# Kernel optimization log

Measured on AMD Instinct MI355X. Metric: run time of the kernel, lower is better.

The kernel has to match this reference:

```python
import jax, jax.numpy as jnp
import numpy as np

ALPHA = 0.2  # LeakyReLU negative slope
NEG_INF = -9e15


def setup_inputs() -> dict:
    key = jax.random.key(0)
    k1, k2, k3, k4 = jax.random.split(key, 4)
    B, T, N, F_in, F_out = 8, 8, 1024, 64, 64
    h = jax.random.normal(k1, (B, T, N, F_in), dtype=jnp.float32)
    adj = jax.random.randint(k2, (B, T, N, N), 0, 2, dtype=jnp.int32)
    # xavier_uniform with gain=1.414
    def xavier(k, shape, gain=1.414):
        fan_in, fan_out = shape[0], shape[1]
        bound = gain * np.sqrt(6.0 / (fan_in + fan_out))
        return jax.random.uniform(k, shape, jnp.float32, -bound, bound)
    W = xavier(k3, (F_in, F_out))
    a = xavier(k4, (2 * F_out, 1))
    return {"h": h, "adj": adj, "W": W, "a": a}


def reference(h, adj, W, a):
    # h: [B,T,N,F_in], adj: [B,T,N,N], W: [F_in,F_out], a: [2*F_out,1]
    F_out = W.shape[1]
    Wh = h @ W  # [B,T,N,F_out]
    a1 = a[:F_out, 0]   # source half
    a2 = a[F_out:, 0]   # target half
    s1 = Wh @ a1        # [B,T,N]
    s2 = Wh @ a2        # [B,T,N]
    # e[...,i,j] = LeakyReLU(s1_i + s2_j)  == original concat-linear score
    e = jax.nn.leaky_relu(s1[..., :, None] + s2[..., None, :], negative_slope=ALPHA)
    att = jnp.where(adj > 0, e, NEG_INF)
    att = jax.nn.softmax(att, axis=-1)  # [B,T,N,N]
    # dropout omitted: reference runs in eval mode (p only active in training)
    h_prime = att @ Wh  # [B,T,N,F_out]
    return jax.nn.elu(h_prime)  # concat=True path
```

## Files before the change

### kernel.cpp

```cpp
#include <hip/hip_runtime.h>

#define NN 1024
#define FF 64
#define NBT 64

typedef float f32x4 __attribute__((ext_vector_type(4)));
typedef short s16x8 __attribute__((ext_vector_type(8)));

__device__ __forceinline__ short f2bf(float f) {
    unsigned u = __builtin_bit_cast(unsigned, f);
    u = (u + 0x7FFFu + ((u >> 16) & 1u)) >> 16;
    return (short)u;
}

__global__ __launch_bounds__(256) void k1(const float* __restrict__ h,
                                          const float* __restrict__ W,
                                          const float* __restrict__ a,
                                          short* __restrict__ WhT,
                                          float* __restrict__ s1g,
                                          float* __restrict__ s2g) {
    __shared__ float Wl[64 * 64];
    __shared__ float al[128];
    __shared__ float s1sh[128], s2sh[128];
    const int blk = blockIdx.x;
    const int bt = blk >> 3;
    const int rbase = (blk & 7) * 128;
    const int t = threadIdx.x;

    for (int i = t; i < 1024; i += 256)
        ((f32x4*)Wl)[i] = ((const f32x4*)W)[i];
    if (t < 32) ((f32x4*)al)[t] = ((const f32x4*)a)[t];
    __syncthreads();

    const int row = rbase + (t & 127);
    const int half = t >> 7;
    const float* hrow = h + ((size_t)bt * NN + row) * FF;
    float hv[64];
#pragma unroll
    for (int i = 0; i < 16; i++)
        ((f32x4*)hv)[i] = ((const f32x4*)hrow)[i];

    float s1 = 0.f, s2 = 0.f;
    short* wt = WhT + (size_t)bt * FF * NN + row;
#pragma unroll
    for (int cgi = 0; cgi < 8; cgi++) {
        const int cg = half * 8 + cgi;
        f32x4 acc = {0.f, 0.f, 0.f, 0.f};
#pragma unroll
        for (int k = 0; k < 64; k++) {
            f32x4 w4 = ((const f32x4*)Wl)[k * 16 + cg];
            acc += hv[k] * w4;
        }
        const int c0 = cg * 4;
        s1 += acc.x * al[c0] + acc.y * al[c0 + 1] + acc.z * al[c0 + 2] + acc.w * al[c0 + 3];
        s2 += acc.x * al[64 + c0] + acc.y * al[64 + c0 + 1] + acc.z * al[64 + c0 + 2] + acc.w * al[64 + c0 + 3];
        wt[(size_t)(c0 + 0) * NN] = f2bf(acc.x);
        wt[(size_t)(c0 + 1) * NN] = f2bf(acc.y);
        wt[(size_t)(c0 + 2) * NN] = f2bf(acc.z);
        wt[(size_t)(c0 + 3) * NN] = f2bf(acc.w);
    }
    if (half == 1) { s1sh[t & 127] = s1; s2sh[t & 127] = s2; }
    __syncthreads();
    if (half == 0) {
        s1g[bt * NN + row] = s1 + s1sh[t];
        s2g[bt * NN + row] = s2 + s2sh[t];
    }
}

__global__ __launch_bounds__(256) void k2(const int* __restrict__ adj,
                                          const short* __restrict__ WhT,
                                          const float* __restrict__ s1g,
                                          const float* __restrict__ s2g,
                                          float* __restrict__ out) {
    __shared__ __align__(16) short Pa[64 * 40];
    __shared__ __align__(16) short Pw[64 * 40];
    __shared__ float s2l[NN];
    __shared__ float rsum[64];

    const int bx = blockIdx.x;
    const int bt = bx >> 4;
    const int ibase = (bx & 15) * 64;
    const int t = threadIdx.x;

    ((f32x4*)s2l)[t] = ((const f32x4*)(s2g + bt * NN))[t];

    const int r = t >> 2;
    const int jc = (t & 3) * 8;
    const float s1v = s1g[bt * NN + ibase + r];
    float rs = 0.f;

    const int* adjp = adj + ((size_t)bt * NN + ibase + r) * NN + jc;
    const short* whp = WhT + (size_t)bt * FF * NN + (size_t)r * NN + jc;

    const int wv = t >> 6;
    const int l = t & 63;
    const int m = l & 15;
    const int q = l >> 4;
    const s16x8* aptr = (const s16x8*)&Pa[(wv * 16 + m) * 40 + q * 8];
    const s16x8* bp0 = (const s16x8*)&Pw[(0 * 16 + m) * 40 + q * 8];
    const s16x8* bp1 = (const s16x8*)&Pw[(1 * 16 + m) * 40 + q * 8];
    const s16x8* bp2 = (const s16x8*)&Pw[(2 * 16 + m) * 40 + q * 8];
    const s16x8* bp3 = (const s16x8*)&Pw[(3 * 16 + m) * 40 + q * 8];

    f32x4 acc0 = {0.f, 0.f, 0.f, 0.f};
    f32x4 acc1 = {0.f, 0.f, 0.f, 0.f};
    f32x4 acc2 = {0.f, 0.f, 0.f, 0.f};
    f32x4 acc3 = {0.f, 0.f, 0.f, 0.f};

    int4 ca0 = *(const int4*)(adjp);
    int4 ca1 = *(const int4*)(adjp + 4);
    int4 cw  = *(const int4*)(whp);

    __syncthreads();

    for (int jt = 0; jt < 32; jt++) {
        const int jn = (jt < 31) ? jt + 1 : 31;
        int4 na0 = *(const int4*)(adjp + jn * 32);
        int4 na1 = *(const int4*)(adjp + jn * 32 + 4);
        int4 nw  = *(const int4*)(whp + jn * 32);

        int aj[8] = {ca0.x, ca0.y, ca0.z, ca0.w, ca1.x, ca1.y, ca1.z, ca1.w};
        f32x4 s2a = *(const f32x4*)&s2l[jt * 32 + jc];
        f32x4 s2b = *(const f32x4*)&s2l[jt * 32 + jc + 4];
        float sv[8] = {s2a.x, s2a.y, s2a.z, s2a.w, s2b.x, s2b.y, s2b.z, s2b.w};
        s16x8 pbv;
#pragma unroll
        for (int u = 0; u < 8; u++) {
            float e = s1v + sv[u];
            e = e > 0.f ? e : 0.2f * e;
            e = fminf(e, 60.f);
            float p = (aj[u] > 0) ? __expf(e) : 0.f;
            rs += p;
            pbv[u] = f2bf(p);
        }
        *(s16x8*)&Pa[r * 40 + jc] = pbv;
        *(int4*)&Pw[r * 40 + jc] = cw;
        __syncthreads();

        s16x8 af = *aptr;
        acc0 = __builtin_amdgcn_mfma_f32_16x16x32_bf16(af, *bp0, acc0, 0, 0, 0);
        acc1 = __builtin_amdgcn_mfma_f32_16x16x32_bf16(af, *bp1, acc1, 0, 0, 0);
        acc2 = __builtin_amdgcn_mfma_f32_16x16x32_bf16(af, *bp2, acc2, 0, 0, 0);
        acc3 = __builtin_amdgcn_mfma_f32_16x16x32_bf16(af, *bp3, acc3, 0, 0, 0);
        __syncthreads();

        ca0 = na0; ca1 = na1; cw = nw;
    }

    rs += __shfl_xor(rs, 1);
    rs += __shfl_xor(rs, 2);
    if ((t & 3) == 0) rsum[r] = rs;
    __syncthreads();

    float rinv[4];
#pragma unroll
    for (int e = 0; e < 4; e++) {
        float rv = rsum[wv * 16 + q * 4 + e];
        rinv[e] = rv > 0.f ? 1.f / rv : 0.f;
    }
    float* outp = out + ((size_t)bt * NN + ibase + wv * 16 + q * 4) * FF + m;
#pragma unroll
    for (int e = 0; e < 4; e++) {
        float v0 = acc0[e] * rinv[e];
        float v1 = acc1[e] * rinv[e];
        float v2 = acc2[e] * rinv[e];
        float v3 = acc3[e] * rinv[e];
        v0 = v0 > 0.f ? v0 : expm1f(v0);
        v1 = v1 > 0.f ? v1 : expm1f(v1);
        v2 = v2 > 0.f ? v2 : expm1f(v2);
        v3 = v3 > 0.f ? v3 : expm1f(v3);
        float* o = outp + (size_t)e * FF;
        o[0]  = v0;
        o[16] = v1;
        o[32] = v2;
        o[48] = v3;
    }
}

extern "C" void kernel_launch(void* const* d_in, const int* in_sizes, int n_in,
                              void* d_out, int out_size, void* d_ws, size_t ws_size,
                              hipStream_t stream) {
    const float* h  = (const float*)d_in[0];
    const int*  adj = (const int*)d_in[1];
    const float* W  = (const float*)d_in[2];
    const float* a  = (const float*)d_in[3];
    float* out = (float*)d_out;

    short* WhT = (short*)d_ws;
    float* s1  = (float*)((char*)d_ws + (size_t)NBT * FF * NN * 2);
    float* s2  = s1 + NBT * NN;

    k1<<<512, 256, 0, stream>>>(h, W, a, WhT, s1, s2);
    k2<<<1024, 256, 0, stream>>>(adj, WhT, s1, s2, out);
}
```

Measured before the change: 415.7 us.

## Load MFMA operands directly into registers, removing LDS staging and barriers

Each lane now computes its attention probabilities directly in the MFMA A-operand layout and loads its WhT B-fragments straight from global memory. This removes the shared-memory staging of P and Wh and the two block barriers per iteration, and the row sums are reduced with wave shuffles instead of through LDS. In exchange, each wave now loads all 64 columns of Wh itself, four times the previous Wh traffic. The adj loads are now strided by row per lane, which may coalesce worse.

New measurement: 421.0 us. No clear change (+1.3%).

```diff
diff --git a/kernel.cpp b/kernel.cpp
--- a/kernel.cpp
+++ b/kernel.cpp
@@ -72,90 +72,80 @@
                                           const float* __restrict__ s1g,
                                           const float* __restrict__ s2g,
                                           float* __restrict__ out) {
-    __shared__ __align__(16) short Pa[64 * 40];
-    __shared__ __align__(16) short Pw[64 * 40];
     __shared__ float s2l[NN];
-    __shared__ float rsum[64];
 
     const int bx = blockIdx.x;
     const int bt = bx >> 4;
     const int ibase = (bx & 15) * 64;
     const int t = threadIdx.x;
-
-    ((f32x4*)s2l)[t] = ((const f32x4*)(s2g + bt * NN))[t];
-
-    const int r = t >> 2;
-    const int jc = (t & 3) * 8;
-    const float s1v = s1g[bt * NN + ibase + r];
-    float rs = 0.f;
-
-    const int* adjp = adj + ((size_t)bt * NN + ibase + r) * NN + jc;
-    const short* whp = WhT + (size_t)bt * FF * NN + (size_t)r * NN + jc;
-
     const int wv = t >> 6;
     const int l = t & 63;
     const int m = l & 15;
     const int q = l >> 4;
-    const s16x8* aptr = (const s16x8*)&Pa[(wv * 16 + m) * 40 + q * 8];
-    const s16x8* bp0 = (const s16x8*)&Pw[(0 * 16 + m) * 40 + q * 8];
-    const s16x8* bp1 = (const s16x8*)&Pw[(1 * 16 + m) * 40 + q * 8];
-    const s16x8* bp2 = (const s16x8*)&Pw[(2 * 16 + m) * 40 + q * 8];
-    const s16x8* bp3 = (const s16x8*)&Pw[(3 * 16 + m) * 40 + q * 8];
+
+    ((f32x4*)s2l)[t] = ((const f32x4*)(s2g + (size_t)bt * NN))[t];
+
+    const int row = ibase + wv * 16 + m;
+    const float s1v = s1g[bt * NN + row];
+
+    const int* adjp = adj + ((size_t)bt * NN + row) * NN + q * 8;
+    const short* whp = WhT + (size_t)bt * FF * NN + (size_t)m * NN + q * 8;
 
     f32x4 acc0 = {0.f, 0.f, 0.f, 0.f};
     f32x4 acc1 = {0.f, 0.f, 0.f, 0.f};
     f32x4 acc2 = {0.f, 0.f, 0.f, 0.f};
     f32x4 acc3 = {0.f, 0.f, 0.f, 0.f};
+    float rs = 0.f;
 
     int4 ca0 = *(const int4*)(adjp);
     int4 ca1 = *(const int4*)(adjp + 4);
-    int4 cw  = *(const int4*)(whp);
+    s16x8 cb0 = *(const s16x8*)(whp);
+    s16x8 cb1 = *(const s16x8*)(whp + 16 * NN);
+    s16x8 cb2 = *(const s16x8*)(whp + 32 * NN);
+    s16x8 cb3 = *(const s16x8*)(whp + 48 * NN);
 
     __syncthreads();
 
     for (int jt = 0; jt < 32; jt++) {
-        const int jn = (jt < 31) ? jt + 1 : 31;
-        int4 na0 = *(const int4*)(adjp + jn * 32);
-        int4 na1 = *(const int4*)(adjp + jn * 32 + 4);
-        int4 nw  = *(const int4*)(whp + jn * 32);
+        const int jn = (jt < 31) ? (jt + 1) * 32 : 31 * 32;
+        int4 na0 = *(const int4*)(adjp + jn);
+        int4 na1 = *(const int4*)(adjp + jn + 4);
+        s16x8 nb0 = *(const s16x8*)(whp + jn);
+        s16x8 nb1 = *(const s16x8*)(whp + 16 * NN + jn);
+        s16x8 nb2 = *(const s16x8*)(whp + 32 * NN + jn);
+        s16x8 nb3 = *(const s16x8*)(whp + 48 * NN + jn);
 
+        f32x4 s2a = *(const f32x4*)&s2l[jt * 32 + q * 8];
+        f32x4 s2b = *(const f32x4*)&s2l[jt * 32 + q * 8 + 4];
         int aj[8] = {ca0.x, ca0.y, ca0.z, ca0.w, ca1.x, ca1.y, ca1.z, ca1.w};
-        f32x4 s2a = *(const f32x4*)&s2l[jt * 32 + jc];
-        f32x4 s2b = *(const f32x4*)&s2l[jt * 32 + jc + 4];
         float sv[8] = {s2a.x, s2a.y, s2a.z, s2a.w, s2b.x, s2b.y, s2b.z, s2b.w};
-        s16x8 pbv;
+        s16x8 af;
 #pragma unroll
         for (int u = 0; u < 8; u++) {
             float e = s1v + sv[u];
-            e = e > 0.f ? e : 0.2f * e;
+            e = fmaxf(e, 0.2f * e);
             e = fminf(e, 60.f);
             float p = (aj[u] > 0) ? __expf(e) : 0.f;
             rs += p;
-            pbv[u] = f2bf(p);
+            af[u] = f2bf(p);
         }
-        *(s16x8*)&Pa[r * 40 + jc] = pbv;
-        *(int4*)&Pw[r * 40 + jc] = cw;
-        __syncthreads();
 
-        s16x8 af = *aptr;
-        acc0 = __builtin_amdgcn_mfma_f32_16x16x32_bf16(af, *bp0, acc0, 0, 0, 0);
-        acc1 = __builtin_amdgcn_mfma_f32_16x16x32_bf16(af, *bp1, acc1, 0, 0, 0);
-        acc2 = __builtin_amdgcn_mfma_f32_16x16x32_bf16(af, *bp2, acc2, 0, 0, 0);
-        acc3 = __builtin_amdgcn_mfma_f32_16x16x32_bf16(af, *bp3, acc3, 0, 0, 0);
-        __syncthreads();
+        acc0 = __builtin_amdgcn_mfma_f32_16x16x32_bf16(af, cb0, acc0, 0, 0, 0);
+        acc1 = __builtin_amdgcn_mfma_f32_16x16x32_bf16(af, cb1, acc1, 0, 0, 0);
+        acc2 = __builtin_amdgcn_mfma_f32_16x16x32_bf16(af, cb2, acc2, 0, 0, 0);
+        acc3 = __builtin_amdgcn_mfma_f32_16x16x32_bf16(af, cb3, acc3, 0, 0, 0);
 
-        ca0 = na0; ca1 = na1; cw = nw;
+        ca0 = na0; ca1 = na1;
+        cb0 = nb0; cb1 = nb1; cb2 = nb2; cb3 = nb3;
     }
 
-    rs += __shfl_xor(rs, 1);
-    rs += __shfl_xor(rs, 2);
-    if ((t & 3) == 0) rsum[r] = rs;
-    __syncthreads();
+    rs += __shfl_xor(rs, 16);
+    rs += __shfl_xor(rs, 32);
 
     float rinv[4];
 #pragma unroll
     for (int e = 0; e < 4; e++) {
-        float rv = rsum[wv * 16 + q * 4 + e];
+        float rv = __shfl(rs, q * 4 + e);
         rinv[e] = rv > 0.f ? 1.f / rv : 0.f;
     }
     float* outp = out + ((size_t)bt * NN + ibase + wv * 16 + q * 4) * FF + m;
```

## Double-buffer LDS tiles, compute row sums via MFMA, use exp2 and remap blocks

Applied to the files above, without the earlier changes.

Double-buffers the P and Wh LDS tiles so the second barrier per iteration can be dropped, and moves the next-tile global loads after the barrier. Row sums now come from an extra MFMA against a ones vector, replacing the scalar accumulation, shuffle reduction and shared-memory pass; these sums are of bf16-rounded probabilities, so numerator and denominator use the same rounding. Scores are prescaled by 1/ln2 in k1 so k2 can use exp2f, with the clamp raised to match. Block indices are also remapped to interleave batch/time slices across the grid.

Measured after the change: 415.5 us. About the same (-0.0%).

```diff
diff --git a/kernel.cpp b/kernel.cpp
--- a/kernel.cpp
+++ b/kernel.cpp
@@ -3,6 +3,7 @@
 #define NN 1024
 #define FF 64
 #define NBT 64
+#define INV_LN2 1.44269504088896f
 
 typedef float f32x4 __attribute__((ext_vector_type(4)));
 typedef short s16x8 __attribute__((ext_vector_type(8)));
@@ -62,8 +63,8 @@
     if (half == 1) { s1sh[t & 127] = s1; s2sh[t & 127] = s2; }
     __syncthreads();
     if (half == 0) {
-        s1g[bt * NN + row] = s1 + s1sh[t];
-        s2g[bt * NN + row] = s2 + s2sh[t];
+        s1g[bt * NN + row] = (s1 + s1sh[t]) * INV_LN2;
+        s2g[bt * NN + row] = (s2 + s2sh[t]) * INV_LN2;
     }
 }
 
@@ -72,22 +73,21 @@
                                           const float* __restrict__ s1g,
                                           const float* __restrict__ s2g,
                                           float* __restrict__ out) {
-    __shared__ __align__(16) short Pa[64 * 40];
-    __shared__ __align__(16) short Pw[64 * 40];
+    __shared__ __align__(16) short Pa[2][64 * 40];
+    __shared__ __align__(16) short Pw[2][64 * 40];
     __shared__ float s2l[NN];
-    __shared__ float rsum[64];
 
-    const int bx = blockIdx.x;
+    const int bxl = blockIdx.x;
+    const int bx = (bxl & 7) * 128 + (bxl >> 3);
     const int bt = bx >> 4;
     const int ibase = (bx & 15) * 64;
     const int t = threadIdx.x;
 
-    ((f32x4*)s2l)[t] = ((const f32x4*)(s2g + bt * NN))[t];
+    ((f32x4*)s2l)[t] = ((const f32x4*)(s2g + (size_t)bt * NN))[t];
 
     const int r = t >> 2;
     const int jc = (t & 3) * 8;
     const float s1v = s1g[bt * NN + ibase + r];
-    float rs = 0.f;
 
     const int* adjp = adj + ((size_t)bt * NN + ibase + r) * NN + jc;
     const short* whp = WhT + (size_t)bt * FF * NN + (size_t)r * NN + jc;
@@ -96,16 +96,18 @@
     const int l = t & 63;
     const int m = l & 15;
     const int q = l >> 4;
-    const s16x8* aptr = (const s16x8*)&Pa[(wv * 16 + m) * 40 + q * 8];
-    const s16x8* bp0 = (const s16x8*)&Pw[(0 * 16 + m) * 40 + q * 8];
-    const s16x8* bp1 = (const s16x8*)&Pw[(1 * 16 + m) * 40 + q * 8];
-    const s16x8* bp2 = (const s16x8*)&Pw[(2 * 16 + m) * 40 + q * 8];
-    const s16x8* bp3 = (const s16x8*)&Pw[(3 * 16 + m) * 40 + q * 8];
+    const int foff = (wv * 16 + m) * 40 + q * 8;
+    const int boff0 = (0 * 16 + m) * 40 + q * 8;
+    const int boff1 = (1 * 16 + m) * 40 + q * 8;
+    const int boff2 = (2 * 16 + m) * 40 + q * 8;
+    const int boff3 = (3 * 16 + m) * 40 + q * 8;
 
     f32x4 acc0 = {0.f, 0.f, 0.f, 0.f};
     f32x4 acc1 = {0.f, 0.f, 0.f, 0.f};
     f32x4 acc2 = {0.f, 0.f, 0.f, 0.f};
     f32x4 acc3 = {0.f, 0.f, 0.f, 0.f};
+    f32x4 accR = {0.f, 0.f, 0.f, 0.f};
+    const s16x8 ones = {0x3F80, 0x3F80, 0x3F80, 0x3F80, 0x3F80, 0x3F80, 0x3F80, 0x3F80};
 
     int4 ca0 = *(const int4*)(adjp);
     int4 ca1 = *(const int4*)(adjp + 4);
@@ -114,10 +116,7 @@
     __syncthreads();
 
     for (int jt = 0; jt < 32; jt++) {
-        const int jn = (jt < 31) ? jt + 1 : 31;
-        int4 na0 = *(const int4*)(adjp + jn * 32);
-        int4 na1 = *(const int4*)(adjp + jn * 32 + 4);
-        int4 nw  = *(const int4*)(whp + jn * 32);
+        const int b = jt & 1;
 
         int aj[8] = {ca0.x, ca0.y, ca0.z, ca0.w, ca1.x, ca1.y, ca1.z, ca1.w};
         f32x4 s2a = *(const f32x4*)&s2l[jt * 32 + jc];
@@ -127,37 +126,35 @@
 #pragma unroll
         for (int u = 0; u < 8; u++) {
             float e = s1v + sv[u];
-            e = e > 0.f ? e : 0.2f * e;
-            e = fminf(e, 60.f);
-            float p = (aj[u] > 0) ? __expf(e) : 0.f;
-            rs += p;
+            e = fmaxf(e, 0.2f * e);
+            e = fminf(e, 86.f);
+            float p = (aj[u] > 0) ? exp2f(e) : 0.f;
             pbv[u] = f2bf(p);
         }
-        *(s16x8*)&Pa[r * 40 + jc] = pbv;
-        *(int4*)&Pw[r * 40 + jc] = cw;
+        *(s16x8*)&Pa[b][r * 40 + jc] = pbv;
+        *(int4*)&Pw[b][r * 40 + jc] = cw;
         __syncthreads();
 
-        s16x8 af = *aptr;
-        acc0 = __builtin_amdgcn_mfma_f32_16x16x32_bf16(af, *bp0, acc0, 0, 0, 0);
-        acc1 = __builtin_amdgcn_mfma_f32_16x16x32_bf16(af, *bp1, acc1, 0, 0, 0);
-        acc2 = __builtin_amdgcn_mfma_f32_16x16x32_bf16(af, *bp2, acc2, 0, 0, 0);
-        acc3 = __builtin_amdgcn_mfma_f32_16x16x32_bf16(af, *bp3, acc3, 0, 0, 0);
-        __syncthreads();
+        const int jn = (jt < 31 ? jt + 1 : 31) * 32;
+        int4 na0 = *(const int4*)(adjp + jn);
+        int4 na1 = *(const int4*)(adjp + jn + 4);
+        int4 nw  = *(const int4*)(whp + jn);
+
+        s16x8 af = *(const s16x8*)&Pa[b][foff];
+        acc0 = __builtin_amdgcn_mfma_f32_16x16x32_bf16(af, *(const s16x8*)&Pw[b][boff0], acc0, 0, 0, 0);
+        acc1 = __builtin_amdgcn_mfma_f32_16x16x32_bf16(af, *(const s16x8*)&Pw[b][boff1], acc1, 0, 0, 0);
+        acc2 = __builtin_amdgcn_mfma_f32_16x16x32_bf16(af, *(const s16x8*)&Pw[b][boff2], acc2, 0, 0, 0);
+        acc3 = __builtin_amdgcn_mfma_f32_16x16x32_bf16(af, *(const s16x8*)&Pw[b][boff3], acc3, 0, 0, 0);
+        accR = __builtin_amdgcn_mfma_f32_16x16x32_bf16(af, ones, accR, 0, 0, 0);
 
         ca0 = na0; ca1 = na1; cw = nw;
     }
 
-    rs += __shfl_xor(rs, 1);
-    rs += __shfl_xor(rs, 2);
-    if ((t & 3) == 0) rsum[r] = rs;
-    __syncthreads();
-
     float rinv[4];
 #pragma unroll
-    for (int e = 0; e < 4; e++) {
-        float rv = rsum[wv * 16 + q * 4 + e];
-        rinv[e] = rv > 0.f ? 1.f / rv : 0.f;
-    }
+    for (int e = 0; e < 4; e++)
+        rinv[e] = accR[e] > 0.f ? 1.f / accR[e] : 0.f;
+
     float* outp = out + ((size_t)bt * NN + ibase + wv * 16 + q * 4) * FF + m;
 #pragma unroll
     for (int e = 0; e < 4; e++) {
```
